# Kernel tuning notes

Measured on AMD Instinct MI355X. Metric: run time of the kernel, lower is better.

The kernel has to match this reference:

```python
import jax, jax.numpy as jnp
import numpy as np
from math import sqrt

B, S, D, H = 2, 2048, 1024, 16
HD = D // H


def setup_inputs() -> dict:
    key = jax.random.key(0)
    ks = jax.random.split(key, 5)
    std = 0.02
    return {
        "tensor_in": jax.random.normal(ks[0], (B, S, D), dtype=jnp.float32),
        "attention_mask": jnp.zeros((1, 1, S, S), dtype=jnp.float32),
        "Wq": jax.random.normal(ks[1], (D, D), dtype=jnp.float32) * std,
        "Wk": jax.random.normal(ks[2], (D, D), dtype=jnp.float32) * std,
        "Wv": jax.random.normal(ks[3], (D, D), dtype=jnp.float32) * std,
        "Wo": jax.random.normal(ks[4], (D, D), dtype=jnp.float32) * std,
    }


def reference(tensor_in, attention_mask, Wq, Wk, Wv, Wo):
    # nn.Linear(dim, dim, bias=False): y = x @ W.T, W is [out, in]
    q = tensor_in @ Wq.T  # [B,S,D]
    k = tensor_in @ Wk.T
    v = tensor_in @ Wv.T
    # split heads -> [B,H,S,HD]
    q = q.reshape(B, S, H, HD).transpose(0, 2, 1, 3)
    k = k.reshape(B, S, H, HD).transpose(0, 2, 1, 3)
    v = v.reshape(B, S, H, HD).transpose(0, 2, 1, 3)
    # scores [B,H,S,S]; note: mask added BEFORE scaling, scale = sqrt(full dim)
    scores = jnp.einsum("bhqd,bhkd->bhqk", q, k) + attention_mask
    weights = jax.nn.softmax(scores / sqrt(D), axis=-1)  # dropout = identity (eval)
    context = jnp.einsum("bhqk,bhkd->bhqd", weights, v)
    context = context.transpose(0, 2, 1, 3).reshape(B, S, D)
    return context @ Wo.T
```

## Files before the change

### kernel.cpp

```cpp
#include <hip/hip_runtime.h>

#define B_  2
#define S_  2048
#define D_  1024
#define H_  16
#define HD_ 64
#define M_  (B_*S_)

typedef __attribute__((ext_vector_type(8))) short  short8;
typedef __attribute__((ext_vector_type(4))) float  float4v;
typedef __attribute__((ext_vector_type(4))) int    int4v;
typedef __attribute__((ext_vector_type(4))) unsigned short ushort4v;

#define PSCALE 0.0450843341f

__device__ __forceinline__ unsigned int pack2_bf16(float a, float b) {
#if __has_builtin(__builtin_amdgcn_cvt_pk_bf16_f32)
    auto p = __builtin_amdgcn_cvt_pk_bf16_f32(a, b);
    return __builtin_bit_cast(unsigned int, p);
#else
    unsigned int xa = __builtin_bit_cast(unsigned int, a);
    unsigned int xb = __builtin_bit_cast(unsigned int, b);
    xa += 0x7fffu + ((xa >> 16) & 1u);
    xb += 0x7fffu + ((xb >> 16) & 1u);
    return (xa >> 16) | (xb & 0xffff0000u);
#endif
}
__device__ __forceinline__ unsigned short f_to_bf16bits(float f) {
#if __has_builtin(__builtin_amdgcn_cvt_pk_bf16_f32)
    return (unsigned short)(pack2_bf16(f, f) & 0xffffu);
#else
    unsigned int x = __builtin_bit_cast(unsigned int, f);
    x += 0x7fffu + ((x >> 16) & 1u);
    return (unsigned short)(x >> 16);
#endif
}

__device__ __forceinline__ float fast_exp2(float x) {
#if __has_builtin(__builtin_amdgcn_exp2f)
    return __builtin_amdgcn_exp2f(x);
#else
    return exp2f(x);
#endif
}

__global__ __launch_bounds__(256) void cvt_bf16(
    const float* __restrict__ X,  const float* __restrict__ Wq,
    const float* __restrict__ Wk, const float* __restrict__ Wv,
    const float* __restrict__ Wo,
    unsigned short* __restrict__ Xb,  unsigned short* __restrict__ Wqb,
    unsigned short* __restrict__ Wkb, unsigned short* __restrict__ Wvb,
    unsigned short* __restrict__ Wob)
{
    const long t = (long)blockIdx.x * 256 + threadIdx.x;
    const long e = t * 8;
    const float* src; unsigned short* dst; long off;
    if      (e < 4194304) { src = X;  dst = Xb;  off = e; }
    else if (e < 5242880) { src = Wq; dst = Wqb; off = e - 4194304; }
    else if (e < 6291456) { src = Wk; dst = Wkb; off = e - 5242880; }
    else if (e < 7340032) { src = Wv; dst = Wvb; off = e - 6291456; }
    else                  { src = Wo; dst = Wob; off = e - 7340032; }
    float4v a = *(const float4v*)&src[off];
    float4v b = *(const float4v*)&src[off + 4];
    int4v o;
    o[0] = (int)pack2_bf16(a[0], a[1]);
    o[1] = (int)pack2_bf16(a[2], a[3]);
    o[2] = (int)pack2_bf16(b[0], b[1]);
    o[3] = (int)pack2_bf16(b[2], b[3]);
    *(int4v*)&dst[off] = o;
}

__global__ __launch_bounds__(256) void gemm_bt(
    const unsigned short* __restrict__ A,
    const unsigned short* __restrict__ B0,
    const unsigned short* __restrict__ B1,
    const unsigned short* __restrict__ B2,
    void* __restrict__ O0, void* __restrict__ O1, void* __restrict__ O2,
    int mode_base)
{
    const int K = 1024;
    const int z = blockIdx.z;
    const int mode = mode_base + z;
    const unsigned short* Aop;
    const unsigned short* Bop;
    void* Op = (z == 0) ? O0 : (z == 1) ? O1 : O2;
    int m0, n0;
    if (mode == 2) {
        Aop = B2; Bop = A;
        m0 = blockIdx.y * 128;
        n0 = blockIdx.x * 128;
    } else {
        Aop = A;
        Bop = (z == 0) ? B0 : (z == 1) ? B1 : B2;
        m0 = blockIdx.x * 128;
        n0 = blockIdx.y * 128;
    }

    __shared__ alignas(16) unsigned short As[128 * 64];
    __shared__ alignas(16) unsigned short Bs[128 * 64];

    const int tid  = threadIdx.x;
    const int wv   = tid >> 6;
    const int lane = tid & 63;
    const int wm   = wv >> 1, wn = wv & 1;
    const int q4   = lane >> 4, l15 = lane & 15;

    const unsigned short* gA[4];
    const unsigned short* gB[4];
    int ldsoff[4];
#pragma unroll
    for (int j = 0; j < 4; j++) {
        const int r = wv * 32 + j * 8 + (lane >> 3);
        const int c = (((lane & 7) ^ (r & 7)) * 8);
        gA[j] = Aop + (long)(m0 + r) * K + c;
        gB[j] = Bop + (long)(n0 + r) * K + c;
        ldsoff[j] = (wv * 32 + j * 8) * 64 + lane * 8;
    }

    int aoff[2][4], boff[2][4];
#pragma unroll
    for (int ks = 0; ks < 2; ks++)
#pragma unroll
        for (int t = 0; t < 4; t++) {
            const int swz = (((ks * 4 + q4) ^ (l15 & 7)) * 8);
            aoff[ks][t] = (wm * 64 + t * 16 + l15) * 64 + swz;
            boff[ks][t] = (wn * 64 + t * 16 + l15) * 64 + swz;
        }

    float4v acc[4][4];
#pragma unroll
    for (int i = 0; i < 4; i++)
#pragma unroll
        for (int j = 0; j < 4; j++) acc[i][j] = (float4v)0.0f;

    int4v ar[4], br[4];
#pragma unroll
    for (int j = 0; j < 4; j++) {
        ar[j] = *(const int4v*)gA[j];
        br[j] = *(const int4v*)gB[j];
        gA[j] += 64; gB[j] += 64;
    }

    for (int k0 = 0; k0 < K; k0 += 64) {
        __syncthreads();
#pragma unroll
        for (int j = 0; j < 4; j++) {
            *(int4v*)&As[ldsoff[j]] = ar[j];
            *(int4v*)&Bs[ldsoff[j]] = br[j];
        }
        __syncthreads();

        if (k0 + 64 < K) {
#pragma unroll
            for (int j = 0; j < 4; j++) {
                ar[j] = *(const int4v*)gA[j];
                br[j] = *(const int4v*)gB[j];
                gA[j] += 64; gB[j] += 64;
            }
        }

#pragma unroll
        for (int ks = 0; ks < 2; ks++) {
            short8 afr[4], bfr[4];
#pragma unroll
            for (int mt = 0; mt < 4; mt++) afr[mt] = *(const short8*)&As[aoff[ks][mt]];
#pragma unroll
            for (int nt = 0; nt < 4; nt++) bfr[nt] = *(const short8*)&Bs[boff[ks][nt]];
#pragma unroll
            for (int mt = 0; mt < 4; mt++)
#pragma unroll
                for (int nt = 0; nt < 4; nt++)
                    acc[mt][nt] = __builtin_amdgcn_mfma_f32_16x16x32_bf16(
                        afr[mt], bfr[nt], acc[mt][nt], 0, 0, 0);
        }
    }

#pragma unroll
    for (int mt = 0; mt < 4; mt++)
#pragma unroll
        for (int nt = 0; nt < 4; nt++)
#pragma unroll
            for (int r = 0; r < 4; r++) {
                const int m = m0 + wm * 64 + mt * 16 + q4 * 4 + r;
                const int n = n0 + wn * 64 + nt * 16 + l15;
                float v = acc[mt][nt][r];
                if (mode == 3) {
                    ((float*)Op)[(long)m * D_ + n] = v;
                } else if (mode == 2) {
                    const long off = (((long)(n >> 11) * H_ + (m >> 6)) * HD_ + (m & 63)) * S_ + (n & 2047);
                    ((unsigned short*)Op)[off] = f_to_bf16bits(v);
                } else {
                    const long off = ((long)((m >> 11) * H_ + (n >> 6)) * S_ + (m & 2047)) * HD_ + (n & 63);
                    if (mode == 0) v *= PSCALE;
                    ((unsigned short*)Op)[off] = f_to_bf16bits(v);
                }
            }
}

__global__ __launch_bounds__(128) void attn(
    const unsigned short* __restrict__ Q,
    const unsigned short* __restrict__ Kk,
    const unsigned short* __restrict__ Vt,
    const float* __restrict__ mask,
    unsigned short* __restrict__ ctx)
{
    __shared__ alignas(16) unsigned short Ks [64 * 72];
    __shared__ alignas(16) unsigned short Vts[64 * 72];
    __shared__ alignas(16) unsigned short Ps [2][32 * 72];

    const int tid  = threadIdx.x;
    const int wv   = tid >> 6;
    const int lane = tid & 63;
    const int q4   = lane >> 4, l15 = lane & 15;
    const int bh   = blockIdx.y;
    const int q0   = blockIdx.x * 64;

    const long head = (long)bh * S_ * HD_;

    short8 qfr[2][2];
#pragma unroll
    for (int mt = 0; mt < 2; mt++) {
        const int qrow = q0 + wv * 32 + mt * 16 + l15;
        qfr[mt][0] = *(const short8*)&Q[head + (long)qrow * HD_ + q4 * 8];
        qfr[mt][1] = *(const short8*)&Q[head + (long)qrow * HD_ + 32 + q4 * 8];
    }

    float l_acc[2][4];
#pragma unroll
    for (int mt = 0; mt < 2; mt++)
#pragma unroll
        for (int r = 0; r < 4; r++) l_acc[mt][r] = 0.0f;
    float4v oacc[2][4];
#pragma unroll
    for (int mt = 0; mt < 2; mt++)
#pragma unroll
        for (int dt = 0; dt < 4; dt++) oacc[mt][dt] = (float4v)0.0f;

    const int srow = tid >> 3;
    const int scol = (tid & 7) * 8;
    const unsigned short* gK[4];
    const unsigned short* gV[4];
    int ldsOff[4];
#pragma unroll
    for (int j = 0; j < 4; j++) {
        const int row = j * 16 + srow;
        gK[j] = Kk + head + (long)row * HD_ + scol;
        gV[j] = Vt + head + (long)row * S_  + scol;
        ldsOff[j] = row * 72 + scol;
    }

    const float* mrow[2][4];
#pragma unroll
    for (int mt = 0; mt < 2; mt++)
#pragma unroll
        for (int r = 0; r < 4; r++)
            mrow[mt][r] = mask + (long)(q0 + wv * 32 + mt * 16 + q4 * 4 + r) * S_ + l15;

    for (int k0 = 0; k0 < S_; k0 += 64) {
        __syncthreads();
#pragma unroll
        for (int j = 0; j < 4; j++) {
            *(int4v*)&Ks [ldsOff[j]] = *(const int4v*)(gK[j] + (long)k0 * HD_);
            *(int4v*)&Vts[ldsOff[j]] = *(const int4v*)(gV[j] + k0);
        }
        __syncthreads();

        float mv[2][4][4];
#pragma unroll
        for (int mt = 0; mt < 2; mt++)
#pragma unroll
            for (int nt = 0; nt < 4; nt++)
#pragma unroll
                for (int r = 0; r < 4; r++)
                    mv[mt][nt][r] = mrow[mt][r][k0 + nt * 16];

        float4v sfr[2][4];
#pragma unroll
        for (int nt = 0; nt < 4; nt++) {
            short8 kb0 = *(const short8*)&Ks[(nt * 16 + l15) * 72 + q4 * 8];
            short8 kb1 = *(const short8*)&Ks[(nt * 16 + l15) * 72 + 32 + q4 * 8];
#pragma unroll
            for (int mt = 0; mt < 2; mt++) {
                float4v s = (float4v)0.0f;
                s = __builtin_amdgcn_mfma_f32_16x16x32_bf16(qfr[mt][0], kb0, s, 0, 0, 0);
                s = __builtin_amdgcn_mfma_f32_16x16x32_bf16(qfr[mt][1], kb1, s, 0, 0, 0);
                sfr[mt][nt] = s;
            }
        }

#pragma unroll
        for (int mt = 0; mt < 2; mt++)
#pragma unroll
            for (int nt = 0; nt < 4; nt++)
#pragma unroll
                for (int r = 0; r < 4; r++) {
                    const float p = fast_exp2(fmaf(mv[mt][nt][r], PSCALE, sfr[mt][nt][r]));
                    l_acc[mt][r] += p;
                    Ps[wv][(mt * 16 + q4 * 4 + r) * 72 + nt * 16 + l15] = f_to_bf16bits(p);
                }

        short8 pf[2][2];
#pragma unroll
        for (int mt = 0; mt < 2; mt++) {
            pf[mt][0] = *(const short8*)&Ps[wv][(mt * 16 + l15) * 72 + q4 * 8];
            pf[mt][1] = *(const short8*)&Ps[wv][(mt * 16 + l15) * 72 + 32 + q4 * 8];
        }

#pragma unroll
        for (int dt = 0; dt < 4; dt++) {
            short8 vb0 = *(const short8*)&Vts[(dt * 16 + l15) * 72 + q4 * 8];
            short8 vb1 = *(const short8*)&Vts[(dt * 16 + l15) * 72 + 32 + q4 * 8];
#pragma unroll
            for (int mt = 0; mt < 2; mt++) {
                float4v o = oacc[mt][dt];
                o = __builtin_amdgcn_mfma_f32_16x16x32_bf16(pf[mt][0], vb0, o, 0, 0, 0);
                o = __builtin_amdgcn_mfma_f32_16x16x32_bf16(pf[mt][1], vb1, o, 0, 0, 0);
                oacc[mt][dt] = o;
            }
        }
    }

#pragma unroll
    for (int mt = 0; mt < 2; mt++)
#pragma unroll
        for (int r = 0; r < 4; r++) {
#pragma unroll
            for (int off = 1; off < 16; off <<= 1)
                l_acc[mt][r] += __shfl_xor(l_acc[mt][r], off);
        }

    const int b = bh >> 4, h = bh & 15;
#pragma unroll
    for (int mt = 0; mt < 2; mt++)
#pragma unroll
        for (int dt = 0; dt < 4; dt++)
#pragma unroll
            for (int r = 0; r < 4; r++) {
                const int qg = q0 + wv * 32 + mt * 16 + q4 * 4 + r;
                const int d  = dt * 16 + l15;
                const float v = oacc[mt][dt][r] / l_acc[mt][r];
                ctx[((long)(b * S_ + qg)) * D_ + h * HD_ + d] = f_to_bf16bits(v);
            }
}

extern "C" void kernel_launch(void* const* d_in, const int* in_sizes, int n_in,
                              void* d_out, int out_size, void* d_ws, size_t ws_size,
                              hipStream_t stream) {
    const float* X    = (const float*)d_in[0];
    const float* mask = (const float*)d_in[1];
    const float* Wq   = (const float*)d_in[2];
    const float* Wk   = (const float*)d_in[3];
    const float* Wv   = (const float*)d_in[4];
    const float* Wo   = (const float*)d_in[5];
    float* out        = (float*)d_out;

    unsigned short* ws = (unsigned short*)d_ws;
    unsigned short* qws  = ws;
    unsigned short* kws  = ws + 4194304;
    unsigned short* vtws = ws + 8388608;
    unsigned short* ctx  = ws + 12582912;
    unsigned short* Xb   = ws + 16777216;
    unsigned short* Wqb  = ws + 20971520;
    unsigned short* Wkb  = ws + 22020096;
    unsigned short* Wvb  = ws + 23068672;
    unsigned short* Wob  = ws + 24117248;

    cvt_bf16<<<dim3(4096), 256, 0, stream>>>(X, Wq, Wk, Wv, Wo, Xb, Wqb, Wkb, Wvb, Wob);
    gemm_bt<<<dim3(32, 8, 3), 256, 0, stream>>>(Xb, Wqb, Wkb, Wvb, qws, kws, vtws, 0);
    attn<<<dim3(32, 32, 1), 128, 0, stream>>>(qws, kws, vtws, mask, ctx);
    gemm_bt<<<dim3(32, 8, 1), 256, 0, stream>>>(ctx, Wob, Wob, Wob, out, out, out, 3);
}
```

Measured before the change: 223.8 us.

## Split attention KV range across two wave pairs and swizzle LDS layout

The attention block grows from 2 to 4 waves. Each pair of waves processes half of the key sequence for the same 64 queries, and the partial output and row sums are combined through shared memory at the end. LDS tiles move from padded 72-element rows to 64-element rows with an XOR swizzle, which saves shared memory while aiming to avoid bank conflicts. The goal is more waves per block for better latency hiding, at the cost of an extra reduction step and higher LDS and register pressure per block.

```diff
diff --git a/kernel.cpp b/kernel.cpp
--- a/kernel.cpp
+++ b/kernel.cpp
@@ -197,30 +197,34 @@
             }
 }
 
-__global__ __launch_bounds__(128) void attn(
+__global__ __launch_bounds__(256) void attn(
     const unsigned short* __restrict__ Q,
     const unsigned short* __restrict__ Kk,
     const unsigned short* __restrict__ Vt,
     const float* __restrict__ mask,
     unsigned short* __restrict__ ctx)
 {
-    __shared__ alignas(16) unsigned short Ks [64 * 72];
-    __shared__ alignas(16) unsigned short Vts[64 * 72];
-    __shared__ alignas(16) unsigned short Ps [2][32 * 72];
+    __shared__ alignas(16) unsigned short SMEM[24576];
 
     const int tid  = threadIdx.x;
     const int wv   = tid >> 6;
+    const int pr   = wv >> 1;
     const int lane = tid & 63;
     const int q4   = lane >> 4, l15 = lane & 15;
     const int bh   = blockIdx.y;
     const int q0   = blockIdx.x * 64;
 
+    unsigned short* Ks  = SMEM + pr * 4096;
+    unsigned short* Vts = SMEM + 8192 + pr * 4096;
+    unsigned short* Ps  = SMEM + 16384 + wv * 2048;
+
     const long head = (long)bh * S_ * HD_;
 
+    const int qbase = (wv & 1) * 32;
     short8 qfr[2][2];
 #pragma unroll
     for (int mt = 0; mt < 2; mt++) {
-        const int qrow = q0 + wv * 32 + mt * 16 + l15;
+        const int qrow = q0 + qbase + mt * 16 + l15;
         qfr[mt][0] = *(const short8*)&Q[head + (long)qrow * HD_ + q4 * 8];
         qfr[mt][1] = *(const short8*)&Q[head + (long)qrow * HD_ + 32 + q4 * 8];
     }
@@ -236,17 +240,19 @@
 #pragma unroll
         for (int dt = 0; dt < 4; dt++) oacc[mt][dt] = (float4v)0.0f;
 
-    const int srow = tid >> 3;
-    const int scol = (tid & 7) * 8;
+    const int ptid = tid & 127;
+    const int srow = ptid >> 3;
+    const int sch  = ptid & 7;
     const unsigned short* gK[4];
     const unsigned short* gV[4];
     int ldsOff[4];
 #pragma unroll
     for (int j = 0; j < 4; j++) {
         const int row = j * 16 + srow;
-        gK[j] = Kk + head + (long)row * HD_ + scol;
-        gV[j] = Vt + head + (long)row * S_  + scol;
-        ldsOff[j] = row * 72 + scol;
+        const int gc  = ((sch ^ (row & 7)) * 8);
+        gK[j] = Kk + head + (long)row * HD_ + gc;
+        gV[j] = Vt + head + (long)row * S_  + gc;
+        ldsOff[j] = row * 64 + sch * 8;
     }
 
     const float* mrow[2][4];
@@ -254,9 +260,15 @@
     for (int mt = 0; mt < 2; mt++)
 #pragma unroll
         for (int r = 0; r < 4; r++)
-            mrow[mt][r] = mask + (long)(q0 + wv * 32 + mt * 16 + q4 * 4 + r) * S_ + l15;
-
-    for (int k0 = 0; k0 < S_; k0 += 64) {
+            mrow[mt][r] = mask + (long)(q0 + qbase + mt * 16 + q4 * 4 + r) * S_ + l15;
+
+    const int pswz = (q4 & 1) * 4;
+    const int psl3 = l15 >> 3;
+    const int kp0 = ((q4       ^ (l15 & 7)) * 8);
+    const int kp1 = (((4 + q4) ^ (l15 & 7)) * 8);
+
+    const int kbeg = pr * 1024, kend = kbeg + 1024;
+    for (int k0 = kbeg; k0 < kend; k0 += 64) {
         __syncthreads();
 #pragma unroll
         for (int j = 0; j < 4; j++) {
@@ -277,8 +289,9 @@
         float4v sfr[2][4];
 #pragma unroll
         for (int nt = 0; nt < 4; nt++) {
-            short8 kb0 = *(const short8*)&Ks[(nt * 16 + l15) * 72 + q4 * 8];
-            short8 kb1 = *(const short8*)&Ks[(nt * 16 + l15) * 72 + 32 + q4 * 8];
+            const int row = nt * 16 + l15;
+            short8 kb0 = *(const short8*)&Ks[row * 64 + ((q4       ^ (row & 7)) * 8)];
+            short8 kb1 = *(const short8*)&Ks[row * 64 + (((4 + q4) ^ (row & 7)) * 8)];
 #pragma unroll
             for (int mt = 0; mt < 2; mt++) {
                 float4v s = (float4v)0.0f;
@@ -296,20 +309,22 @@
                 for (int r = 0; r < 4; r++) {
                     const float p = fast_exp2(fmaf(mv[mt][nt][r], PSCALE, sfr[mt][nt][r]));
                     l_acc[mt][r] += p;
-                    Ps[wv][(mt * 16 + q4 * 4 + r) * 72 + nt * 16 + l15] = f_to_bf16bits(p);
+                    const int c8 = (nt * 2 + psl3) ^ (pswz + r);
+                    Ps[(mt * 16 + q4 * 4 + r) * 64 + c8 * 8 + (l15 & 7)] = f_to_bf16bits(p);
                 }
 
         short8 pf[2][2];
 #pragma unroll
         for (int mt = 0; mt < 2; mt++) {
-            pf[mt][0] = *(const short8*)&Ps[wv][(mt * 16 + l15) * 72 + q4 * 8];
-            pf[mt][1] = *(const short8*)&Ps[wv][(mt * 16 + l15) * 72 + 32 + q4 * 8];
+            pf[mt][0] = *(const short8*)&Ps[(mt * 16 + l15) * 64 + kp0];
+            pf[mt][1] = *(const short8*)&Ps[(mt * 16 + l15) * 64 + kp1];
         }
 
 #pragma unroll
         for (int dt = 0; dt < 4; dt++) {
-            short8 vb0 = *(const short8*)&Vts[(dt * 16 + l15) * 72 + q4 * 8];
-            short8 vb1 = *(const short8*)&Vts[(dt * 16 + l15) * 72 + 32 + q4 * 8];
+            const int row = dt * 16 + l15;
+            short8 vb0 = *(const short8*)&Vts[row * 64 + ((q4       ^ (row & 7)) * 8)];
+            short8 vb1 = *(const short8*)&Vts[row * 64 + (((4 + q4) ^ (row & 7)) * 8)];
 #pragma unroll
             for (int mt = 0; mt < 2; mt++) {
                 float4v o = oacc[mt][dt];
@@ -320,27 +335,47 @@
         }
     }
 
-#pragma unroll
-    for (int mt = 0; mt < 2; mt++)
-#pragma unroll
-        for (int r = 0; r < 4; r++) {
-#pragma unroll
-            for (int off = 1; off < 16; off <<= 1)
-                l_acc[mt][r] += __shfl_xor(l_acc[mt][r], off);
-        }
-
-    const int b = bh >> 4, h = bh & 15;
-#pragma unroll
-    for (int mt = 0; mt < 2; mt++)
-#pragma unroll
-        for (int dt = 0; dt < 4; dt++)
+    __syncthreads();
+    float* Osh = (float*)SMEM;
+    float* Lsh = (float*)(SMEM + 16384);
+    if (pr == 1) {
+#pragma unroll
+        for (int mt = 0; mt < 2; mt++) {
+#pragma unroll
+            for (int dt = 0; dt < 4; dt++)
+#pragma unroll
+                for (int r = 0; r < 4; r++)
+                    Osh[(wv & 1) * 2048 + (mt * 16 + q4 * 4 + r) * 64 + dt * 16 + l15] =
+                        oacc[mt][dt][r];
+#pragma unroll
+            for (int r = 0; r < 4; r++)
+                Lsh[(wv & 1) * 512 + ((mt * 4 + r) * 4 + q4) * 16 + l15] = l_acc[mt][r];
+        }
+    }
+    __syncthreads();
+    if (pr == 0) {
+        const int b = bh >> 4, h = bh & 15;
+#pragma unroll
+        for (int mt = 0; mt < 2; mt++) {
 #pragma unroll
             for (int r = 0; r < 4; r++) {
-                const int qg = q0 + wv * 32 + mt * 16 + q4 * 4 + r;
-                const int d  = dt * 16 + l15;
-                const float v = oacc[mt][dt][r] / l_acc[mt][r];
-                ctx[((long)(b * S_ + qg)) * D_ + h * HD_ + d] = f_to_bf16bits(v);
+                l_acc[mt][r] += Lsh[(wv & 1) * 512 + ((mt * 4 + r) * 4 + q4) * 16 + l15];
+#pragma unroll
+                for (int off = 1; off < 16; off <<= 1)
+                    l_acc[mt][r] += __shfl_xor(l_acc[mt][r], off);
             }
+#pragma unroll
+            for (int dt = 0; dt < 4; dt++)
+#pragma unroll
+                for (int r = 0; r < 4; r++) {
+                    const float o2 = Osh[(wv & 1) * 2048 + (mt * 16 + q4 * 4 + r) * 64 + dt * 16 + l15];
+                    const int qg = q0 + qbase + mt * 16 + q4 * 4 + r;
+                    const int d  = dt * 16 + l15;
+                    const float v = (oacc[mt][dt][r] + o2) / l_acc[mt][r];
+                    ctx[((long)(b * S_ + qg)) * D_ + h * HD_ + d] = f_to_bf16bits(v);
+                }
+        }
+    }
 }
 
 extern "C" void kernel_launch(void* const* d_in, const int* in_sizes, int n_in,
@@ -367,6 +402,6 @@
 
     cvt_bf16<<<dim3(4096), 256, 0, stream>>>(X, Wq, Wk, Wv, Wo, Xb, Wqb, Wkb, Wvb, Wob);
     gemm_bt<<<dim3(32, 8, 3), 256, 0, stream>>>(Xb, Wqb, Wkb, Wvb, qws, kws, vtws, 0);
-    attn<<<dim3(32, 32, 1), 128, 0, stream>>>(qws, kws, vtws, mask, ctx);
+    attn<<<dim3(32, 32, 1), 256, 0, stream>>>(qws, kws, vtws, mask, ctx);
     gemm_bt<<<dim3(32, 8, 1), 256, 0, stream>>>(ctx, Wob, Wob, Wob, out, out, out, 3);
 }
```

Measured after the change: 236.7 us. +5.8%, slower.
